# Kernel tuning notes

Hardware: AMD Instinct MI355X
Metric: run time of the kernel (lower is better)

## Reference

```python
import jax, jax.numpy as jnp
import numpy as np

B, K, IN_DIM, H, D = 8, 4096, 512, 8, 64  # batch, tokens, in_dim, heads, per-head dim


def setup_inputs() -> dict:
    key = jax.random.key(0)
    ks = jax.random.split(key, 8)
    s = 0.02
    return {
        "x": jax.random.normal(ks[0], (B, K, IN_DIM), jnp.float32),
        "y": jax.random.normal(ks[1], (B, K, IN_DIM), jnp.float32),
        "Wq": jax.random.normal(ks[2], (IN_DIM, H * D), jnp.float32) * s,
        "bq": jnp.zeros((H * D,), jnp.float32),
        "Wk": jax.random.normal(ks[3], (IN_DIM, H * D), jnp.float32) * s,
        "bk": jnp.zeros((H * D,), jnp.float32),
        "Wv": jax.random.normal(ks[4], (IN_DIM, H * D), jnp.float32) * s,
        "bv": jnp.zeros((H * D,), jnp.float32),
        "Wp": jax.random.normal(ks[5], (IN_DIM, D), jnp.float32) * s,
        "gamma": jax.random.uniform(ks[6], (H, 1, 1, 1), jnp.float32) + 0.001,
    }


def _heads(t):
    # (B, K, H*D) -> (H, B, K, D); matches split_cat(t, D, dim=2, cat dim=0) head-major layout
    b, k, _ = t.shape
    return t.reshape(b, k, H, D).transpose(2, 0, 1, 3)


def reference(x, y, Wq, bq, Wk, bk, Wv, bv, Wp, gamma):
    q = _heads(x @ Wq + bq)   # (H,B,K,D)
    kk = _heads(x @ Wk + bk)  # (H,B,K,D)
    v = _heads(y @ Wv + bv)   # (H,B,K,D)
    # energy = q^T k contracted over tokens -> (H,B,D,D)
    energy = jnp.einsum('hbkd,hbke->hbde', q, kk)
    attn = jax.nn.softmax(energy, axis=-1)
    # out = v @ attn^T : out[k,q] = sum_e v[k,e] * attn[q,e]
    out = jnp.einsum('hbke,hbqe->hbkq', v, attn)  # (H,B,K,D)
    yp = y @ Wp  # projection(y): (B,K,D)
    out = (gamma * out + yp[None]) / (1.0 + gamma)
    return out.transpose(1, 0, 2, 3)  # (B,H,K,D)
```

## Files before the change

kernel.cpp:

```cpp
#include <hip/hip_runtime.h>

#define B_ 8
#define K_ 4096
#define IN_ 512
#define H_ 8
#define D_ 64
#define HD_ 512

typedef short bf16x8 __attribute__((ext_vector_type(8)));
typedef float f32x4 __attribute__((ext_vector_type(4)));
typedef unsigned short u16;
typedef unsigned short us8v __attribute__((ext_vector_type(8)));
typedef unsigned short us4v __attribute__((ext_vector_type(4)));

__device__ inline u16 f2bf_rn(float f) {
  unsigned u = __float_as_uint(f);
  u += 0x7fffu + ((u >> 16) & 1u);
  return (u16)(u >> 16);
}
__device__ inline float bf2f(u16 h) {
  return __uint_as_float(((unsigned)h) << 16);
}

__device__ inline void gl_lds16(const u16* g, u16* l) {
  __builtin_amdgcn_global_load_lds(
      (const __attribute__((address_space(1))) unsigned int*)g,
      (__attribute__((address_space(3))) unsigned int*)l, 16, 0, 0);
}


__global__ __launch_bounds__(256) void k_cvt_x(const float* __restrict__ x,
                                               u16* __restrict__ xt_hi,
                                               u16* __restrict__ xt_lo,
                                               float* __restrict__ svec) {
  const int kt = blockIdx.x, ct = blockIdx.y, b = blockIdx.z;
  __shared__ float Xs[64][65];
  const int tid = threadIdx.x;
  const float* src = x + ((size_t)b * K_ + kt * 64) * IN_ + ct * 64;
#pragma unroll
  for (int r = 0; r < 4; ++r) {
    int idx = tid + 256 * r;
    int k = idx >> 4, c4 = (idx & 15) * 4;
    f32x4 v = *(const f32x4*)(src + (size_t)k * IN_ + c4);
    Xs[k][c4 + 0] = v[0];
    Xs[k][c4 + 1] = v[1];
    Xs[k][c4 + 2] = v[2];
    Xs[k][c4 + 3] = v[3];
  }
  __syncthreads();
  if (tid < 64) {
    float s = 0.f;
#pragma unroll
    for (int k = 0; k < 64; ++k) s += Xs[k][tid];
    atomicAdd(&svec[b * IN_ + ct * 64 + tid], s);
  }
#pragma unroll
  for (int r = 0; r < 2; ++r) {
    int idx = tid + 256 * r;
    int c = idx >> 3, ck = (idx & 7) * 8;
    us8v hv, lv;
#pragma unroll
    for (int j = 0; j < 8; ++j) {
      float f = Xs[ck + j][c];
      u16 h = f2bf_rn(f);
      float lo = f - bf2f(h);
      hv[j] = h;
      lv[j] = f2bf_rn(lo);
    }
    size_t off = ((size_t)(b * IN_ + ct * 64 + c)) * K_ + kt * 64 + ck;
    *(us8v*)(xt_hi + off) = hv;
    *(us8v*)(xt_lo + off) = lv;
  }
}

__global__ __launch_bounds__(256) void k_cvt_y(const float* __restrict__ y,
                                               u16* __restrict__ yb) {
  size_t i = ((size_t)blockIdx.x * 256 + threadIdx.x) * 8;
  f32x4 v0 = *(const f32x4*)(y + i);
  f32x4 v1 = *(const f32x4*)(y + i + 4);
  us8v o;
  o[0] = f2bf_rn(v0[0]); o[1] = f2bf_rn(v0[1]);
  o[2] = f2bf_rn(v0[2]); o[3] = f2bf_rn(v0[3]);
  o[4] = f2bf_rn(v1[0]); o[5] = f2bf_rn(v1[1]);
  o[6] = f2bf_rn(v1[2]); o[7] = f2bf_rn(v1[3]);
  *(us8v*)(yb + i) = o;
}

__global__ __launch_bounds__(256) void k_cvt_w(
    const float* __restrict__ Wq, const float* __restrict__ Wk,
    u16* __restrict__ Wqt_hi, u16* __restrict__ Wqt_lo,
    u16* __restrict__ Wkt_hi, u16* __restrict__ Wkt_lo) {
  const int ti = blockIdx.x, tj = blockIdx.y;
  const float* src = blockIdx.z ? Wk : Wq;
  u16* dhi = blockIdx.z ? Wkt_hi : Wqt_hi;
  u16* dlo = blockIdx.z ? Wkt_lo : Wqt_lo;
  __shared__ float T[64][65];
  const int tid = threadIdx.x;
#pragma unroll
  for (int r = 0; r < 4; ++r) {
    int idx = tid + 256 * r;
    int rr = idx >> 4, c4 = (idx & 15) * 4;
    f32x4 v = *(const f32x4*)(src + (size_t)(tj * 64 + rr) * 512 + ti * 64 + c4);
    T[rr][c4 + 0] = v[0]; T[rr][c4 + 1] = v[1];
    T[rr][c4 + 2] = v[2]; T[rr][c4 + 3] = v[3];
  }
  __syncthreads();
#pragma unroll
  for (int r = 0; r < 2; ++r) {
    int idx = tid + 256 * r;
    int d = idx >> 3, ck = (idx & 7) * 8;
    us8v hv, lv;
#pragma unroll
    for (int j = 0; j < 8; ++j) {
      float f = T[ck + j][d];
      u16 h = f2bf_rn(f);
      hv[j] = h;
      lv[j] = f2bf_rn(f - bf2f(h));
    }
    size_t off = (size_t)(ti * 64 + d) * 512 + tj * 64 + ck;
    *(us8v*)(dhi + off) = hv;
    *(us8v*)(dlo + off) = lv;
  }
}

#define GP 72

__global__ __launch_bounds__(256, 2) void k_gram_mfma(
    const u16* __restrict__ xt_hi, const u16* __restrict__ xt_lo,
    float* __restrict__ G) {
  const int fid = blockIdx.x;
  const int kc = fid & 7;
  const int slot = fid >> 3;
  const int b = slot / 10;
  int pp = slot - b * 10, ti = 0;
  while (pp >= 4 - ti) { pp -= 4 - ti; ++ti; }
  const int tj = ti + pp;
  const bool diag = (ti == tj);
  __shared__ u16 P[2][4 * 128 * 32];
  const int tid = threadIdx.x;
  const int wave = tid >> 6, lane = tid & 63;
  const int wm = wave & 1, wn = wave >> 1;
  const int m16 = lane & 15, quad = lane >> 4;
  const size_t base_i = ((size_t)(b * IN_ + ti * 128)) * K_;
  const size_t base_j = ((size_t)(b * IN_ + tj * 128)) * K_;
  const int sr = lane >> 2, sslot = lane & 3;
  const int boff_h = diag ? 0 : 2 * 4096;
  const int boff_l = diag ? 4096 : 3 * 4096;

  f32x4 zf = {0.f, 0.f, 0.f, 0.f};
  f32x4 acc[4][4];
#pragma unroll
  for (int mt = 0; mt < 4; ++mt)
#pragma unroll
    for (int nt = 0; nt < 4; ++nt) acc[mt][nt] = zf;
  const int kbeg = kc * 512;

  auto STAGE = [&](int t, int buf) {
    const int k0 = kbeg + t * 32;
    u16* Pb = &P[buf][0];
#pragma unroll
    for (int g = 0; g < 2; ++g) {
      int rbase = wave * 32 + g * 16;
      int r = rbase + sr;
      size_t go = (size_t)r * K_ + k0 + ((sslot ^ ((sr >> 1) & 3)) << 3);
      int lo = rbase * 32;
      gl_lds16(xt_hi + base_i + go, Pb + 0 * 4096 + lo);
      gl_lds16(xt_lo + base_i + go, Pb + 1 * 4096 + lo);
      if (!diag) {
        gl_lds16(xt_hi + base_j + go, Pb + 2 * 4096 + lo);
        gl_lds16(xt_lo + base_j + go, Pb + 3 * 4096 + lo);
      }
    }
  };

  STAGE(0, 0);
  int cur = 0;
  const int ac = ((quad ^ ((m16 >> 1) & 3)) << 3);
  for (int t = 0; t < 16; ++t) {
    if (t < 15) {
      STAGE(t + 1, cur ^ 1);
      if (diag) asm volatile("s_waitcnt vmcnt(4)" ::: "memory");
      else      asm volatile("s_waitcnt vmcnt(8)" ::: "memory");
    } else {
      asm volatile("s_waitcnt vmcnt(0)" ::: "memory");
    }
    __builtin_amdgcn_s_barrier();
    __builtin_amdgcn_sched_barrier(0);
    const u16* Pb = &P[cur][0];
    bf16x8 ah[4], al[4], bh[4], bl[4];
#pragma unroll
    for (int tt = 0; tt < 4; ++tt) {
      int ar = (wm * 64 + tt * 16 + m16) * 32 + ac;
      ah[tt] = *(const bf16x8*)(Pb + ar);
      al[tt] = *(const bf16x8*)(Pb + 4096 + ar);
      int br = (wn * 64 + tt * 16 + m16) * 32 + ac;
      bh[tt] = *(const bf16x8*)(Pb + boff_h + br);
      bl[tt] = *(const bf16x8*)(Pb + boff_l + br);
    }
#pragma unroll
    for (int mt = 0; mt < 4; ++mt)
#pragma unroll
      for (int nt = 0; nt < 4; ++nt) {
        acc[mt][nt] = __builtin_amdgcn_mfma_f32_16x16x32_bf16(
            ah[mt], bh[nt], acc[mt][nt], 0, 0, 0);
        acc[mt][nt] = __builtin_amdgcn_mfma_f32_16x16x32_bf16(
            ah[mt], bl[nt], acc[mt][nt], 0, 0, 0);
        acc[mt][nt] = __builtin_amdgcn_mfma_f32_16x16x32_bf16(
            al[mt], bh[nt], acc[mt][nt], 0, 0, 0);
      }
    __builtin_amdgcn_s_barrier();
    cur ^= 1;
  }
  float* Gb = G + (size_t)b * IN_ * IN_;
#pragma unroll
  for (int mt = 0; mt < 4; ++mt)
#pragma unroll
    for (int nt = 0; nt < 4; ++nt)
#pragma unroll
      for (int r = 0; r < 4; ++r) {
        int gi = ti * 128 + wm * 64 + mt * 16 + quad * 4 + r;
        int gj = tj * 128 + wn * 64 + nt * 16 + m16;
        atomicAdd(&Gb[(size_t)gi * IN_ + gj], acc[mt][nt][r]);
      }
}

__global__ __launch_bounds__(256) void k_cvt_g(const float* __restrict__ G,
                                               u16* __restrict__ Ghi,
                                               u16* __restrict__ Glo) {
  const int ti = blockIdx.x, tj = blockIdx.y, b = blockIdx.z;
  if (tj < ti) return;
  const float* Gb = G + (size_t)b * IN_ * IN_;
  u16* ghb = Ghi + (size_t)b * IN_ * IN_;
  u16* glb = Glo + (size_t)b * IN_ * IN_;
  __shared__ float T[64][65];
  const int tid = threadIdx.x;
#pragma unroll
  for (int r = 0; r < 4; ++r) {
    int idx = tid + 256 * r;
    int rr = idx >> 4, c4 = (idx & 15) * 4;
    f32x4 v = *(const f32x4*)(Gb + (size_t)(ti * 64 + rr) * IN_ + tj * 64 + c4);
    T[rr][c4 + 0] = v[0]; T[rr][c4 + 1] = v[1];
    T[rr][c4 + 2] = v[2]; T[rr][c4 + 3] = v[3];
  }
  __syncthreads();
#pragma unroll
  for (int r = 0; r < 2; ++r) {
    int idx = tid + 256 * r;
    int rr = idx >> 3, ck = (idx & 7) * 8;
    us8v hv, lv;
#pragma unroll
    for (int j = 0; j < 8; ++j) {
      float f = T[rr][ck + j];
      u16 h = f2bf_rn(f);
      hv[j] = h;
      lv[j] = f2bf_rn(f - bf2f(h));
    }
    size_t off = (size_t)(ti * 64 + rr) * IN_ + tj * 64 + ck;
    *(us8v*)(ghb + off) = hv;
    *(us8v*)(glb + off) = lv;
  }
  if (ti != tj) {
#pragma unroll
    for (int r = 0; r < 2; ++r) {
      int idx = tid + 256 * r;
      int rr = idx >> 3, ck = (idx & 7) * 8;
      us8v hv, lv;
#pragma unroll
      for (int j = 0; j < 8; ++j) {
        float f = T[ck + j][rr];
        u16 h = f2bf_rn(f);
        hv[j] = h;
        lv[j] = f2bf_rn(f - bf2f(h));
      }
      size_t off = (size_t)(tj * 64 + rr) * IN_ + ti * 64 + ck;
      *(us8v*)(ghb + off) = hv;
      *(us8v*)(glb + off) = lv;
    }
  }
}

__global__ __launch_bounds__(256) void k_aall_mfma(
    const u16* __restrict__ Wqt_hi, const u16* __restrict__ Wqt_lo,
    const u16* __restrict__ Ghi, const u16* __restrict__ Glo,
    u16* __restrict__ Ahi, u16* __restrict__ Alo) {
  const int ct = blockIdx.x;
  const int hb = blockIdx.y;
  const int h = hb >> 3, b = hb & 7;
  __shared__ u16 S[4 * 64 * 64];
  u16* Ah = S;
  u16* Al = S + 64 * 64;
  u16* Bh = S + 2 * 64 * 64;
  u16* Bl = S + 3 * 64 * 64;
  const int tid = threadIdx.x;
  const int wave = tid >> 6, lane = tid & 63;
  const int m16 = lane & 15, quad = lane >> 4;
  const u16* Abase_h = Wqt_hi + (size_t)(h * 64) * IN_;
  const u16* Abase_l = Wqt_lo + (size_t)(h * 64) * IN_;
  const u16* Bbase_h = Ghi + (size_t)b * IN_ * IN_ + (size_t)(ct * 64) * IN_;
  const u16* Bbase_l = Glo + (size_t)b * IN_ * IN_ + (size_t)(ct * 64) * IN_;
  const int lrow = lane >> 3;
  const int lcol = ((lane & 7) * 8) ^ (lrow << 3);
  const size_t loff = (size_t)lrow * IN_ + lcol;
  f32x4 zf = {0.f, 0.f, 0.f, 0.f};
  f32x4 acc[4] = {zf, zf, zf, zf};
  for (int k0 = 0; k0 < IN_; k0 += 64) {
    __syncthreads();
#pragma unroll
    for (int r = 0; r < 2; ++r) {
      int rg = wave * 2 + r;
      size_t go = (size_t)(rg * 8) * IN_ + k0 + loff;
      int lo = rg * 8 * 64;
      gl_lds16(Abase_h + go, &Ah[lo]);
      gl_lds16(Abase_l + go, &Al[lo]);
      gl_lds16(Bbase_h + go, &Bh[lo]);
      gl_lds16(Bbase_l + go, &Bl[lo]);
    }
    __syncthreads();
#pragma unroll
    for (int kk = 0; kk < 64; kk += 32) {
      const int ac = (kk + quad * 8) ^ ((m16 & 7) << 3);
      int arow = (wave * 16 + m16) * 64 + ac;
      bf16x8 ah = *(const bf16x8*)&Ah[arow];
      bf16x8 al = *(const bf16x8*)&Al[arow];
#pragma unroll
      for (int n = 0; n < 4; ++n) {
        int brow = (n * 16 + m16) * 64 + ac;
        bf16x8 bh = *(const bf16x8*)&Bh[brow];
        bf16x8 bl = *(const bf16x8*)&Bl[brow];
        acc[n] = __builtin_amdgcn_mfma_f32_16x16x32_bf16(ah, bh, acc[n], 0, 0, 0);
        acc[n] = __builtin_amdgcn_mfma_f32_16x16x32_bf16(ah, bl, acc[n], 0, 0, 0);
        acc[n] = __builtin_amdgcn_mfma_f32_16x16x32_bf16(al, bh, acc[n], 0, 0, 0);
      }
    }
  }
  __syncthreads();
  float* Sf = (float*)S;
#pragma unroll
  for (int n = 0; n < 4; ++n)
#pragma unroll
    for (int r = 0; r < 4; ++r) {
      int d = wave * 16 + quad * 4 + r;
      int cc = n * 16 + m16;
      Sf[d * 68 + cc] = acc[n][r];
    }
  __syncthreads();
#pragma unroll
  for (int r = 0; r < 2; ++r) {
    int idx = tid + 256 * r;
    int d = idx >> 3, ck = (idx & 7) * 8;
    us8v hv, lv;
#pragma unroll
    for (int j = 0; j < 8; ++j) {
      float f = Sf[d * 68 + ck + j];
      u16 h2 = f2bf_rn(f);
      hv[j] = h2;
      lv[j] = f2bf_rn(f - bf2f(h2));
    }
    size_t off = ((size_t)hb * 64 + d) * IN_ + ct * 64 + ck;
    *(us8v*)(Ahi + off) = hv;
    *(us8v*)(Alo + off) = lv;
  }
}

__global__ __launch_bounds__(256) void k_attn3(
    const u16* __restrict__ Ahi, const u16* __restrict__ Alo,
    const u16* __restrict__ Wqt_hi, const u16* __restrict__ Wqt_lo,
    const u16* __restrict__ Wkt_hi, const u16* __restrict__ Wkt_lo,
    const float* __restrict__ Wv, const float* __restrict__ Wp,
    const float* __restrict__ bq, const float* __restrict__ bk,
    const float* __restrict__ bv, const float* __restrict__ gamma,
    const float* __restrict__ svec, u16* __restrict__ Wft,
    float* __restrict__ bfin) {
  const int h = blockIdx.x, b = blockIdx.y;
  const int hb = h * B_ + b;
  const int tid = threadIdx.x;
  const int wave = tid >> 6, lane = tid & 63;
  const int m16 = lane & 15, quad = lane >> 4;
  __shared__ u16 S[4 * 64 * GP];
  __shared__ float Esh[64][65];
  __shared__ float t1[64], t2[64];
  u16* Ah = S;
  u16* Al = S + 64 * GP;
  u16* Bh = S + 2 * 64 * GP;
  u16* Bl = S + 3 * 64 * GP;

  if (tid < 64) {
    float s = 0.f;
    const u16* wh = Wkt_hi + (size_t)(h * 64 + tid) * IN_;
    const u16* wl = Wkt_lo + (size_t)(h * 64 + tid) * IN_;
    const float* sv = svec + b * IN_;
    for (int c = 0; c < IN_; c += 8) {
      us8v hv = *(const us8v*)(wh + c);
      us8v lv = *(const us8v*)(wl + c);
#pragma unroll
      for (int j = 0; j < 8; ++j)
        s += sv[c + j] * (bf2f(hv[j]) + bf2f(lv[j]));
    }
    t1[tid] = s;
  } else if (tid < 128) {
    int d = tid - 64;
    float s = 0.f;
    const u16* wh = Wqt_hi + (size_t)(h * 64 + d) * IN_;
    const u16* wl = Wqt_lo + (size_t)(h * 64 + d) * IN_;
    const float* sv = svec + b * IN_;
    for (int c = 0; c < IN_; c += 8) {
      us8v hv = *(const us8v*)(wh + c);
      us8v lv = *(const us8v*)(wl + c);
#pragma unroll
      for (int j = 0; j < 8; ++j)
        s += sv[c + j] * (bf2f(hv[j]) + bf2f(lv[j]));
    }
    t2[d] = s;
  }

  const u16* Abase_h = Ahi + (size_t)hb * 64 * IN_;
  const u16* Abase_l = Alo + (size_t)hb * 64 * IN_;
  const u16* Bbase_h = Wkt_hi + (size_t)(h * 64) * IN_;
  const u16* Bbase_l = Wkt_lo + (size_t)(h * 64) * IN_;
  f32x4 zf = {0.f, 0.f, 0.f, 0.f};
  f32x4 acc[4] = {zf, zf, zf, zf};
  for (int k0 = 0; k0 < IN_; k0 += 64) {
    __syncthreads();
#pragma unroll
    for (int r = 0; r < 2; ++r) {
      int idx = tid + 256 * r;
      int row = idx >> 3, ck = (idx & 7) * 8;
      int lo = row * GP + ck;
      *(us8v*)&Ah[lo] = *(const us8v*)(Abase_h + (size_t)row * IN_ + k0 + ck);
      *(us8v*)&Al[lo] = *(const us8v*)(Abase_l + (size_t)row * IN_ + k0 + ck);
      *(us8v*)&Bh[lo] = *(const us8v*)(Bbase_h + (size_t)row * IN_ + k0 + ck);
      *(us8v*)&Bl[lo] = *(const us8v*)(Bbase_l + (size_t)row * IN_ + k0 + ck);
    }
    __syncthreads();
#pragma unroll
    for (int kk = 0; kk < 64; kk += 32) {
      int arow = (wave * 16 + m16) * GP + kk + quad * 8;
      bf16x8 ah = *(const bf16x8*)&Ah[arow];
      bf16x8 al = *(const bf16x8*)&Al[arow];
#pragma unroll
      for (int n = 0; n < 4; ++n) {
        int brow = (n * 16 + m16) * GP + kk + quad * 8;
        bf16x8 bh = *(const bf16x8*)&Bh[brow];
        bf16x8 bl = *(const bf16x8*)&Bl[brow];
        acc[n] = __builtin_amdgcn_mfma_f32_16x16x32_bf16(ah, bh, acc[n], 0, 0, 0);
        acc[n] = __builtin_amdgcn_mfma_f32_16x16x32_bf16(ah, bl, acc[n], 0, 0, 0);
        acc[n] = __builtin_amdgcn_mfma_f32_16x16x32_bf16(al, bh, acc[n], 0, 0, 0);
      }
    }
  }
  __syncthreads();
#pragma unroll
  for (int n = 0; n < 4; ++n)
#pragma unroll
    for (int r = 0; r < 4; ++r) {
      int d = wave * 16 + quad * 4 + r;
      int e = n * 16 + m16;
      float bqd = bq[h * D_ + d], bke = bk[h * D_ + e];
      Esh[d][e] = acc[n][r] + bqd * t1[e] + t2[d] * bke + (float)K_ * bqd * bke;
    }
  __syncthreads();
  const float g = gamma[h];
  const float inv1g = 1.f / (1.f + g);
  if (tid < 64) {
    float m = -1e30f;
    for (int e = 0; e < 64; ++e) m = fmaxf(m, Esh[tid][e]);
    float ssum = 0.f;
    for (int e = 0; e < 64; ++e) {
      float p = __expf(Esh[tid][e] - m);
      Esh[tid][e] = p;
      ssum += p;
    }
    float inv = 1.f / ssum;
    float bsum = 0.f;
    for (int e = 0; e < 64; ++e) {
      Esh[tid][e] *= inv;
      bsum += bv[h * D_ + e] * Esh[tid][e];
    }
    bfin[hb * D_ + tid] = g * bsum * inv1g;
  }
  __syncthreads();

  bf16x8 bfr[4][2];
#pragma unroll
  for (int n = 0; n < 4; ++n)
#pragma unroll
    for (int kk = 0; kk < 2; ++kk)
#pragma unroll
      for (int j = 0; j < 8; ++j)
        bfr[n][kk][j] = f2bf_rn(Esh[n * 16 + m16][kk * 32 + quad * 8 + j]);

  u16* Wf = Wft + (size_t)hb * D_ * IN_;
#pragma unroll
  for (int mt = 0; mt < 8; ++mt) {
    f32x4 a4[4] = {zf, zf, zf, zf};
#pragma unroll
    for (int kk = 0; kk < 2; ++kk) {
      int c = wave * 128 + mt * 16 + m16;
      const float* wv = Wv + (size_t)c * HD_ + h * D_ + kk * 32 + quad * 8;
      f32x4 v0 = *(const f32x4*)wv;
      f32x4 v1 = *(const f32x4*)(wv + 4);
      bf16x8 af;
      af[0] = f2bf_rn(v0[0]); af[1] = f2bf_rn(v0[1]);
      af[2] = f2bf_rn(v0[2]); af[3] = f2bf_rn(v0[3]);
      af[4] = f2bf_rn(v1[0]); af[5] = f2bf_rn(v1[1]);
      af[6] = f2bf_rn(v1[2]); af[7] = f2bf_rn(v1[3]);
#pragma unroll
      for (int n = 0; n < 4; ++n)
        a4[n] = __builtin_amdgcn_mfma_f32_16x16x32_bf16(af, bfr[n][kk], a4[n], 0, 0, 0);
    }
    int cb = wave * 128 + mt * 16 + quad * 4;
#pragma unroll
    for (int n = 0; n < 4; ++n) {
      int q = n * 16 + m16;
      us4v st;
#pragma unroll
      for (int r = 0; r < 4; ++r) {
        float val = (g * a4[n][r] + Wp[(size_t)(cb + r) * D_ + q]) * inv1g;
        st[r] = f2bf_rn(val);
      }
      *(us4v*)(Wf + (size_t)q * IN_ + cb) = st;
    }
  }
}

__global__ __launch_bounds__(256, 2) void k_out_mfma(
    const u16* __restrict__ yb, const u16* __restrict__ Wft,
    const float* __restrict__ bfin, float* __restrict__ out) {
  const int kt = blockIdx.x;
  const int b = blockIdx.y & 7, hq = blockIdx.y >> 3;
  const int h0 = hq * 2;
  __shared__ u16 Wsh[2][2 * 64 * 64];
  const int tid = threadIdx.x, wave = tid >> 6, lane = tid & 63;
  const int m16 = lane & 15, quad = lane >> 4;
  const int swz = (m16 & 7) << 3;

  us8v stg[4];
  auto LOAD = [&](int c0) {
#pragma unroll
    for (int r = 0; r < 4; ++r) {
      int idx = tid + 256 * r;
      int row = idx >> 3, ck = (idx & 7) * 8;
      int i = row >> 6, q = row & 63;
      const u16* src =
          Wft + ((size_t)((h0 + i) * 8 + b) * 64 + q) * IN_ + c0 + ck;
      stg[r] = *(const us8v*)src;
    }
  };
  auto WRITE = [&](int buf) {
#pragma unroll
    for (int r = 0; r < 4; ++r) {
      int idx = tid + 256 * r;
      int row = idx >> 3, ck = (idx & 7) * 8;
      *(us8v*)&Wsh[buf][row * 64 + (ck ^ ((row & 7) << 3))] = stg[r];
    }
  };
  bf16x8 yf[2][4];
  auto LOADY = [&](bf16x8 (*yd)[4], int c0) {
#pragma unroll
    for (int kk = 0; kk < 2; ++kk)
#pragma unroll
      for (int ms = 0; ms < 4; ++ms) {
        int row = kt * 256 + wave * 64 + ms * 16 + m16;
        yd[kk][ms] = *(const bf16x8*)(yb + ((size_t)b * K_ + row) * IN_ + c0 +
                                      kk * 32 + quad * 8);
      }
  };

  f32x4 zf = {0.f, 0.f, 0.f, 0.f};
  f32x4 acc[4][2][4];
#pragma unroll
  for (int ms = 0; ms < 4; ++ms)
#pragma unroll
    for (int i = 0; i < 2; ++i)
#pragma unroll
      for (int nt = 0; nt < 4; ++nt) acc[ms][i][nt] = zf;

  LOAD(0);
  LOADY(yf, 0);
  WRITE(0);
  __syncthreads();
  int cur = 0;
  for (int c0 = 0; c0 < IN_; c0 += 64) {
    const bool more = (c0 + 64 < IN_);
    bf16x8 yn[2][4];
    if (more) {
      LOAD(c0 + 64);
      LOADY(yn, c0 + 64);
    }
#pragma unroll
    for (int kk = 0; kk < 2; ++kk)
#pragma unroll
      for (int i = 0; i < 2; ++i)
#pragma unroll
        for (int nt = 0; nt < 4; ++nt) {
          int brow = i * 64 + nt * 16 + m16;
          bf16x8 bb = *(const bf16x8*)&Wsh[cur][brow * 64 +
                                               ((kk * 32 + quad * 8) ^ swz)];
#pragma unroll
          for (int ms = 0; ms < 4; ++ms)
            acc[ms][i][nt] = __builtin_amdgcn_mfma_f32_16x16x32_bf16(
                yf[kk][ms], bb, acc[ms][i][nt], 0, 0, 0);
        }
    if (more) {
      WRITE(cur ^ 1);
      __syncthreads();
      cur ^= 1;
#pragma unroll
      for (int kk = 0; kk < 2; ++kk)
#pragma unroll
        for (int ms = 0; ms < 4; ++ms) yf[kk][ms] = yn[kk][ms];
    }
  }

#pragma unroll
  for (int i = 0; i < 2; ++i) {
    float* ob = out + (((size_t)b * H_ + h0 + i) * K_) * D_;
    const int hb = (h0 + i) * 8 + b;
#pragma unroll
    for (int ms = 0; ms < 4; ++ms)
#pragma unroll
      for (int nt = 0; nt < 4; ++nt) {
        int col = nt * 16 + m16;
        float bf = bfin[hb * D_ + col];
#pragma unroll
        for (int r = 0; r < 4; ++r) {
          int row = kt * 256 + wave * 64 + ms * 16 + quad * 4 + r;
          ob[(size_t)row * D_ + col] = acc[ms][i][nt][r] + bf;
        }
      }
  }
}

__global__ __launch_bounds__(256) void k_gram(const float* __restrict__ x,
                                              float* __restrict__ G,
                                              float* __restrict__ svec) {
  const int it = blockIdx.x, jt = blockIdx.y, b = blockIdx.z;
  if (jt < it) return;
  __shared__ float Xi[16][64];
  __shared__ float Xj[16][64];
  const float* Xb = x + (size_t)b * K_ * IN_;
  const int tx = threadIdx.x, ty = threadIdx.y;
  const int tid = ty * 16 + tx;
  const int i0 = it * 64, j0 = jt * 64;
  const bool diag = (it == jt);
  float acc[4][4] = {};
  float ssum = 0.f;
  for (int k0 = 0; k0 < K_; k0 += 16) {
#pragma unroll
    for (int r = 0; r < 4; ++r) {
      int idx = tid + 256 * r;
      int kk = idx >> 6, cc = idx & 63;
      const float* row = Xb + (size_t)(k0 + kk) * IN_;
      Xi[kk][cc] = row[i0 + cc];
      Xj[kk][cc] = row[j0 + cc];
    }
    __syncthreads();
#pragma unroll
    for (int kk = 0; kk < 16; ++kk) {
      float a[4], bb[4];
#pragma unroll
      for (int u = 0; u < 4; ++u) a[u] = Xi[kk][ty * 4 + u];
#pragma unroll
      for (int u = 0; u < 4; ++u) bb[u] = Xj[kk][tx * 4 + u];
#pragma unroll
      for (int u = 0; u < 4; ++u)
#pragma unroll
        for (int w = 0; w < 4; ++w) acc[u][w] += a[u] * bb[w];
    }
    if (diag && tid < 64) {
#pragma unroll
      for (int kk = 0; kk < 16; ++kk) ssum += Xi[kk][tid];
    }
    __syncthreads();
  }
  float* Gb = G + (size_t)b * IN_ * IN_;
#pragma unroll
  for (int u = 0; u < 4; ++u)
#pragma unroll
    for (int w = 0; w < 4; ++w) {
      int gi = i0 + ty * 4 + u, gj = j0 + tx * 4 + w;
      Gb[(size_t)gi * IN_ + gj] = acc[u][w];
      if (!diag) Gb[(size_t)gj * IN_ + gi] = acc[u][w];
    }
  if (diag && tid < 64) svec[b * IN_ + i0 + tid] = ssum;
}

__global__ __launch_bounds__(256) void k_aall(const float* __restrict__ Wq,
                                              const float* __restrict__ G,
                                              float* __restrict__ Aall) {
  const int jt = blockIdx.x;
  const int h = blockIdx.y, b = blockIdx.z;
  __shared__ float Ws[16][64];
  __shared__ float Gs[16][64];
  const float* Gb = G + (size_t)b * IN_ * IN_;
  const int tx = threadIdx.x, ty = threadIdx.y;
  const int tid = ty * 16 + tx;
  float acc[4][4] = {};
  for (int c0 = 0; c0 < IN_; c0 += 16) {
#pragma unroll
    for (int r = 0; r < 4; ++r) {
      int idx = tid + 256 * r;
      int kk = idx >> 6, cc = idx & 63;
      Ws[kk][cc] = Wq[(size_t)(c0 + kk) * HD_ + h * D_ + cc];
      Gs[kk][cc] = Gb[(size_t)(c0 + kk) * IN_ + jt * 64 + cc];
    }
    __syncthreads();
#pragma unroll
    for (int kk = 0; kk < 16; ++kk) {
      float a[4], bb[4];
#pragma unroll
      for (int u = 0; u < 4; ++u) a[u] = Ws[kk][ty * 4 + u];
#pragma unroll
      for (int u = 0; u < 4; ++u) bb[u] = Gs[kk][tx * 4 + u];
#pragma unroll
      for (int u = 0; u < 4; ++u)
#pragma unroll
        for (int w = 0; w < 4; ++w) acc[u][w] += a[u] * bb[w];
    }
    __syncthreads();
  }
  const int hb = h * B_ + b;
  float* Ahb = Aall + (size_t)hb * D_ * IN_;
#pragma unroll
  for (int u = 0; u < 4; ++u)
#pragma unroll
    for (int w = 0; w < 4; ++w)
      Ahb[(size_t)(ty * 4 + u) * IN_ + jt * 64 + tx * 4 + w] = acc[u][w];
}

__global__ __launch_bounds__(256) void k_attn_f32(
    const float* __restrict__ Wq, const float* __restrict__ Wk,
    const float* __restrict__ Wv, const float* __restrict__ Wp,
    const float* __restrict__ bq, const float* __restrict__ bk,
    const float* __restrict__ bv, const float* __restrict__ gamma,
    const float* __restrict__ Aall, const float* __restrict__ svec,
    float* __restrict__ Wfin, float* __restrict__ bfin) {
  const int h = blockIdx.x, b = blockIdx.y;
  const int hb = h * B_ + b;
  const int tx = threadIdx.x, ty = threadIdx.y;
  const int tid = ty * 16 + tx;
  __shared__ float Ast[64][17];
  __shared__ float Ws[16][64];
  __shared__ float Esh[64][65];
  __shared__ float t1[64], t2[64];
  const float* Ahb = Aall + (size_t)hb * D_ * IN_;
  if (tid < 64) {
    float a2 = 0.f;
    for (int c = 0; c < IN_; ++c)
      a2 += svec[b * IN_ + c] * Wk[(size_t)c * HD_ + h * D_ + tid];
    t1[tid] = a2;
  } else if (tid < 128) {
    int d = tid - 64;
    float a2 = 0.f;
    for (int c = 0; c < IN_; ++c)
      a2 += svec[b * IN_ + c] * Wq[(size_t)c * HD_ + h * D_ + d];
    t2[d] = a2;
  }
  float acc[4][4] = {};
  for (int c0 = 0; c0 < IN_; c0 += 16) {
#pragma unroll
    for (int r = 0; r < 4; ++r) {
      int idx = tid + 256 * r;
      int dd = idx >> 4, kk = idx & 15;
      Ast[dd][kk] = Ahb[(size_t)dd * IN_ + c0 + kk];
      int kk2 = idx >> 6, ee = idx & 63;
      Ws[kk2][ee] = Wk[(size_t)(c0 + kk2) * HD_ + h * D_ + ee];
    }
    __syncthreads();
#pragma unroll
    for (int kk = 0; kk < 16; ++kk) {
      float a[4], bb[4];
#pragma unroll
      for (int u = 0; u < 4; ++u) a[u] = Ast[ty * 4 + u][kk];
#pragma unroll
      for (int u = 0; u < 4; ++u) bb[u] = Ws[kk][tx * 4 + u];
#pragma unroll
      for (int u = 0; u < 4; ++u)
#pragma unroll
        for (int w = 0; w < 4; ++w) acc[u][w] += a[u] * bb[w];
    }
    __syncthreads();
  }
#pragma unroll
  for (int u = 0; u < 4; ++u) {
    int d = ty * 4 + u;
    float bqd = bq[h * D_ + d];
    float t2d = t2[d];
#pragma unroll
    for (int w = 0; w < 4; ++w) {
      int e = tx * 4 + w;
      float bke = bk[h * D_ + e];
      Esh[d][e] = acc[u][w] + bqd * t1[e] + t2d * bke + (float)K_ * bqd * bke;
    }
  }
  __syncthreads();
  if (tid < 64) {
    float m = -1e30f;
    for (int e = 0; e < 64; ++e) m = fmaxf(m, Esh[tid][e]);
    float ssum = 0.f;
    for (int e = 0; e < 64; ++e) {
      float p = __expf(Esh[tid][e] - m);
      Esh[tid][e] = p;
      ssum += p;
    }
    float inv = 1.f / ssum;
    for (int e = 0; e < 64; ++e) Esh[tid][e] *= inv;
  }
  __syncthreads();
  const float g = gamma[h];
  const float inv1g = 1.f / (1.f + g);
  if (tid < 64) {
    float a2 = 0.f;
    for (int e = 0; e < 64; ++e) a2 += bv[h * D_ + e] * Esh[tid][e];
    bfin[hb * D_ + tid] = g * a2 * inv1g;
  }
  float* Wf = Wfin + (size_t)hb * IN_ * D_;
  for (int it2 = 0; it2 < 128; ++it2) {
    int idx = tid + 256 * it2;
    int c = idx >> 6, q = idx & 63;
    const float* Wvr = Wv + (size_t)c * HD_ + h * D_;
    float a2 = 0.f;
#pragma unroll
    for (int e = 0; e < 64; ++e) a2 += Wvr[e] * Esh[q][e];
    Wf[idx] = (g * a2 + Wp[(size_t)c * D_ + q]) * inv1g;
  }
}

__global__ __launch_bounds__(256) void k_out_f32(const float* __restrict__ y,
                                                 const float* __restrict__ Wfin,
                                                 const float* __restrict__ bfin,
                                                 float* __restrict__ out) {
  const int kt = blockIdx.x;
  const int hb = blockIdx.y;
  const int h = hb >> 3, b = hb & 7;
  __shared__ float Ys[64][17];
  __shared__ float Ws[16][64];
  const int tx = threadIdx.x, ty = threadIdx.y;
  const int tid = ty * 16 + tx;
  const float* Yb = y + (size_t)b * K_ * IN_;
  const float* Wf = Wfin + (size_t)hb * IN_ * D_;
  const int k0 = kt * 64;
  float acc[4][4] = {};
  for (int c0 = 0; c0 < IN_; c0 += 16) {
#pragma unroll
    for (int r = 0; r < 4; ++r) {
      int idx = tid + 256 * r;
      int rr = idx >> 4, kk = idx & 15;
      Ys[rr][kk] = Yb[(size_t)(k0 + rr) * IN_ + c0 + kk];
      int kk2 = idx >> 6, qq = idx & 63;
      Ws[kk2][qq] = Wf[(size_t)(c0 + kk2) * D_ + qq];
    }
    __syncthreads();
#pragma unroll
    for (int kk = 0; kk < 16; ++kk) {
      float a[4], bb[4];
#pragma unroll
      for (int u = 0; u < 4; ++u) a[u] = Ys[ty * 4 + u][kk];
#pragma unroll
      for (int u = 0; u < 4; ++u) bb[u] = Ws[kk][tx * 4 + u];
#pragma unroll
      for (int u = 0; u < 4; ++u)
#pragma unroll
        for (int w = 0; w < 4; ++w) acc[u][w] += a[u] * bb[w];
    }
    __syncthreads();
  }
  float* ob = out + (((size_t)b * H_ + h) * K_ + k0) * D_;
#pragma unroll
  for (int u = 0; u < 4; ++u) {
    int k = ty * 4 + u;
#pragma unroll
    for (int w = 0; w < 4; ++w) {
      int q = tx * 4 + w;
      ob[(size_t)k * D_ + q] = acc[u][w] + bfin[hb * D_ + q];
    }
  }
}

extern "C" void kernel_launch(void* const* d_in, const int* in_sizes, int n_in,
                              void* d_out, int out_size, void* d_ws,
                              size_t ws_size, hipStream_t stream) {
  const float* x = (const float*)d_in[0];
  const float* y = (const float*)d_in[1];
  const float* Wq = (const float*)d_in[2];
  const float* bq = (const float*)d_in[3];
  const float* Wk = (const float*)d_in[4];
  const float* bk = (const float*)d_in[5];
  const float* Wv = (const float*)d_in[6];
  const float* bv = (const float*)d_in[7];
  const float* Wp = (const float*)d_in[8];
  const float* gm = (const float*)d_in[9];
  float* out = (float*)d_out;

  const size_t NEED = 86016000;
  if (ws_size >= NEED) {
    char* w = (char*)d_ws;
    u16* xt_hi = (u16*)(w);
    u16* Ahi = (u16*)(w);
    u16* Alo = (u16*)(w + 4194304);
    u16* Wft = (u16*)(w + 8388608);
    u16* xt_lo = (u16*)(w + 33554432);
    u16* yb = (u16*)(w + 33554432);
    float* G = (float*)(w + 67108864);
    u16* Ghi = (u16*)(w + 75497472);
    u16* Glo = (u16*)(w + 79691776);
    u16* Wqt_hi = (u16*)(w + 83886080);
    u16* Wqt_lo = (u16*)(w + 84410368);
    u16* Wkt_hi = (u16*)(w + 84934656);
    u16* Wkt_lo = (u16*)(w + 85458944);
    float* bfin = (float*)(w + 85983232);
    float* svec = (float*)(w + 85999616);

    hipMemsetAsync(G, 0, 8388608, stream);
    hipMemsetAsync(svec, 0, 16384, stream);
    k_cvt_w<<<dim3(8, 8, 2), 256, 0, stream>>>(Wq, Wk, Wqt_hi, Wqt_lo, Wkt_hi,
                                               Wkt_lo);
    k_cvt_x<<<dim3(64, 8, 8), 256, 0, stream>>>(x, xt_hi, xt_lo, svec);
    k_gram_mfma<<<dim3(640), 256, 0, stream>>>(xt_hi, xt_lo, G);
    k_cvt_y<<<dim3(8192), 256, 0, stream>>>(y, yb);
    k_cvt_g<<<dim3(8, 8, 8), 256, 0, stream>>>(G, Ghi, Glo);
    k_aall_mfma<<<dim3(8, 64), 256, 0, stream>>>(Wqt_hi, Wqt_lo, Ghi, Glo, Ahi,
                                                 Alo);
    k_attn3<<<dim3(8, 8), 256, 0, stream>>>(Ahi, Alo, Wqt_hi, Wqt_lo, Wkt_hi,
                                            Wkt_lo, Wv, Wp, bq, bk, bv, gm,
                                            svec, Wft, bfin);
    k_out_mfma<<<dim3(16, 32), 256, 0, stream>>>(yb, Wft, bfin, out);
  } else {
    float* ws = (float*)d_ws;
    float* G = ws;
    float* Aall = ws + 2097152;
    float* Wfin = ws + 4194304;
    float* bfin = ws + 6291456;
    float* svec = ws + 6295552;
    dim3 blk(16, 16);
    k_gram<<<dim3(8, 8, 8), blk, 0, stream>>>(x, G, svec);
    k_aall<<<dim3(8, 8, 8), blk, 0, stream>>>(Wq, G, Aall);
    k_attn_f32<<<dim3(8, 8), blk, 0, stream>>>(Wq, Wk, Wv, Wp, bq, bk, bv, gm,
                                               Aall, svec, Wfin, bfin);
    k_out_f32<<<dim3(64, 64), blk, 0, stream>>>(y, Wfin, bfin, out);
  }
}
```

Measured before the change: 328.4 us.

## Enlarge gram MFMA tiles to 256x256 with 512-thread blocks

The Gram-matrix kernel now computes 256x256 output tiles per block with 8 waves instead of 128x128 with 4 waves, cutting the grid from 640 to 192 blocks. Each wave holds 8x4 accumulator tiles and loads A fragments per row-tile inside the loop, improving operand reuse and lowering redundant global loads per output. The cost is higher register pressure, doubled LDS usage, and fewer blocks to fill the CUs, which may hurt occupancy and load balance.

```diff
diff --git a/kernel.cpp b/kernel.cpp
--- a/kernel.cpp
+++ b/kernel.cpp
@@ -125,32 +125,32 @@
 
 #define GP 72
 
-__global__ __launch_bounds__(256, 2) void k_gram_mfma(
+__global__ __launch_bounds__(512, 2) void k_gram_mfma(
     const u16* __restrict__ xt_hi, const u16* __restrict__ xt_lo,
     float* __restrict__ G) {
   const int fid = blockIdx.x;
   const int kc = fid & 7;
-  const int slot = fid >> 3;
-  const int b = slot / 10;
-  int pp = slot - b * 10, ti = 0;
-  while (pp >= 4 - ti) { pp -= 4 - ti; ++ti; }
-  const int tj = ti + pp;
+  const int sl = fid >> 3;
+  const int b = sl & 7;
+  const int pp = sl >> 3;
+  const int ti = pp >> 1, tj = (pp + 1) >> 1;
   const bool diag = (ti == tj);
-  __shared__ u16 P[2][4 * 128 * 32];
+  __shared__ u16 P[2][4 * 256 * 32];
+  const int AOFF = 256 * 32;
   const int tid = threadIdx.x;
   const int wave = tid >> 6, lane = tid & 63;
   const int wm = wave & 1, wn = wave >> 1;
   const int m16 = lane & 15, quad = lane >> 4;
-  const size_t base_i = ((size_t)(b * IN_ + ti * 128)) * K_;
-  const size_t base_j = ((size_t)(b * IN_ + tj * 128)) * K_;
+  const size_t base_i = ((size_t)(b * IN_ + ti * 256)) * K_;
+  const size_t base_j = ((size_t)(b * IN_ + tj * 256)) * K_;
   const int sr = lane >> 2, sslot = lane & 3;
-  const int boff_h = diag ? 0 : 2 * 4096;
-  const int boff_l = diag ? 4096 : 3 * 4096;
+  const int boff_h = diag ? 0 : 2 * AOFF;
+  const int boff_l = diag ? AOFF : 3 * AOFF;
 
   f32x4 zf = {0.f, 0.f, 0.f, 0.f};
-  f32x4 acc[4][4];
-#pragma unroll
-  for (int mt = 0; mt < 4; ++mt)
+  f32x4 acc[8][4];
+#pragma unroll
+  for (int mt = 0; mt < 8; ++mt)
 #pragma unroll
     for (int nt = 0; nt < 4; ++nt) acc[mt][nt] = zf;
   const int kbeg = kc * 512;
@@ -164,11 +164,11 @@
       int r = rbase + sr;
       size_t go = (size_t)r * K_ + k0 + ((sslot ^ ((sr >> 1) & 3)) << 3);
       int lo = rbase * 32;
-      gl_lds16(xt_hi + base_i + go, Pb + 0 * 4096 + lo);
-      gl_lds16(xt_lo + base_i + go, Pb + 1 * 4096 + lo);
+      gl_lds16(xt_hi + base_i + go, Pb + lo);
+      gl_lds16(xt_lo + base_i + go, Pb + AOFF + lo);
       if (!diag) {
-        gl_lds16(xt_hi + base_j + go, Pb + 2 * 4096 + lo);
-        gl_lds16(xt_lo + base_j + go, Pb + 3 * 4096 + lo);
+        gl_lds16(xt_hi + base_j + go, Pb + 2 * AOFF + lo);
+        gl_lds16(xt_lo + base_j + go, Pb + 3 * AOFF + lo);
       }
     }
   };
@@ -187,39 +187,40 @@
     __builtin_amdgcn_s_barrier();
     __builtin_amdgcn_sched_barrier(0);
     const u16* Pb = &P[cur][0];
-    bf16x8 ah[4], al[4], bh[4], bl[4];
-#pragma unroll
-    for (int tt = 0; tt < 4; ++tt) {
-      int ar = (wm * 64 + tt * 16 + m16) * 32 + ac;
-      ah[tt] = *(const bf16x8*)(Pb + ar);
-      al[tt] = *(const bf16x8*)(Pb + 4096 + ar);
-      int br = (wn * 64 + tt * 16 + m16) * 32 + ac;
-      bh[tt] = *(const bf16x8*)(Pb + boff_h + br);
-      bl[tt] = *(const bf16x8*)(Pb + boff_l + br);
-    }
-#pragma unroll
-    for (int mt = 0; mt < 4; ++mt)
+    bf16x8 bh[4], bl[4];
+#pragma unroll
+    for (int nt = 0; nt < 4; ++nt) {
+      int br = (wn * 64 + nt * 16 + m16) * 32 + ac;
+      bh[nt] = *(const bf16x8*)(Pb + boff_h + br);
+      bl[nt] = *(const bf16x8*)(Pb + boff_l + br);
+    }
+#pragma unroll
+    for (int mt = 0; mt < 8; ++mt) {
+      int ar = (wm * 128 + mt * 16 + m16) * 32 + ac;
+      bf16x8 ah = *(const bf16x8*)(Pb + ar);
+      bf16x8 al = *(const bf16x8*)(Pb + AOFF + ar);
 #pragma unroll
       for (int nt = 0; nt < 4; ++nt) {
         acc[mt][nt] = __builtin_amdgcn_mfma_f32_16x16x32_bf16(
-            ah[mt], bh[nt], acc[mt][nt], 0, 0, 0);
+            ah, bh[nt], acc[mt][nt], 0, 0, 0);
         acc[mt][nt] = __builtin_amdgcn_mfma_f32_16x16x32_bf16(
-            ah[mt], bl[nt], acc[mt][nt], 0, 0, 0);
+            ah, bl[nt], acc[mt][nt], 0, 0, 0);
         acc[mt][nt] = __builtin_amdgcn_mfma_f32_16x16x32_bf16(
-            al[mt], bh[nt], acc[mt][nt], 0, 0, 0);
+            al, bh[nt], acc[mt][nt], 0, 0, 0);
       }
+    }
     __builtin_amdgcn_s_barrier();
     cur ^= 1;
   }
   float* Gb = G + (size_t)b * IN_ * IN_;
 #pragma unroll
-  for (int mt = 0; mt < 4; ++mt)
+  for (int mt = 0; mt < 8; ++mt)
 #pragma unroll
     for (int nt = 0; nt < 4; ++nt)
 #pragma unroll
       for (int r = 0; r < 4; ++r) {
-        int gi = ti * 128 + wm * 64 + mt * 16 + quad * 4 + r;
-        int gj = tj * 128 + wn * 64 + nt * 16 + m16;
+        int gi = ti * 256 + wm * 128 + mt * 16 + quad * 4 + r;
+        int gj = tj * 256 + wn * 64 + nt * 16 + m16;
         atomicAdd(&Gb[(size_t)gi * IN_ + gj], acc[mt][nt][r]);
       }
 }
@@ -916,7 +917,7 @@
     k_cvt_w<<<dim3(8, 8, 2), 256, 0, stream>>>(Wq, Wk, Wqt_hi, Wqt_lo, Wkt_hi,
                                                Wkt_lo);
     k_cvt_x<<<dim3(64, 8, 8), 256, 0, stream>>>(x, xt_hi, xt_lo, svec);
-    k_gram_mfma<<<dim3(640), 256, 0, stream>>>(xt_hi, xt_lo, G);
+    k_gram_mfma<<<dim3(192), 512, 0, stream>>>(xt_hi, xt_lo, G);
     k_cvt_y<<<dim3(8192), 256, 0, stream>>>(y, yb);
     k_cvt_g<<<dim3(8, 8, 8), 256, 0, stream>>>(G, Ghi, Glo);
     k_aall_mfma<<<dim3(8, 64), 256, 0, stream>>>(Wqt_hi, Wqt_lo, Ghi, Glo, Ahi,
```

Measured after the change: 348.9 us. 1.06x slower.

## Split final weight fusion out of attention kernel into wider-grid k_wft

Applied to the files above, without the earlier changes.

The attention kernel now stops after the softmax and writes the bf16 attention matrix to workspace, reusing the Gram buffer region. A new kernel k_wft with a 4x64 grid computes the fused Wv·attn plus Wp weight matrix, splitting the 512 output columns across four blocks per head-batch pair. The aim is to spread the serial MFMA tail, which previously ran on only 64 blocks, across more CUs. The cost is an extra launch plus a small global round trip for the attention matrix.

```diff
diff --git a/kernel.cpp b/kernel.cpp
--- a/kernel.cpp
+++ b/kernel.cpp
@@ -366,10 +366,9 @@
     const u16* __restrict__ Ahi, const u16* __restrict__ Alo,
     const u16* __restrict__ Wqt_hi, const u16* __restrict__ Wqt_lo,
     const u16* __restrict__ Wkt_hi, const u16* __restrict__ Wkt_lo,
-    const float* __restrict__ Wv, const float* __restrict__ Wp,
     const float* __restrict__ bq, const float* __restrict__ bk,
     const float* __restrict__ bv, const float* __restrict__ gamma,
-    const float* __restrict__ svec, u16* __restrict__ Wft,
+    const float* __restrict__ svec, u16* __restrict__ Pbf,
     float* __restrict__ bfin) {
   const int h = blockIdx.x, b = blockIdx.y;
   const int hb = h * B_ + b;
@@ -480,22 +479,49 @@
   }
   __syncthreads();
 
+  {
+    int q = tid >> 2, c0 = (tid & 3) * 16;
+    us8v o1, o2;
+#pragma unroll
+    for (int j = 0; j < 8; ++j) {
+      o1[j] = f2bf_rn(Esh[q][c0 + j]);
+      o2[j] = f2bf_rn(Esh[q][c0 + 8 + j]);
+    }
+    u16* Pq = Pbf + (size_t)hb * 4096 + q * 64 + c0;
+    *(us8v*)Pq = o1;
+    *(us8v*)(Pq + 8) = o2;
+  }
+}
+
+__global__ __launch_bounds__(256) void k_wft(
+    const u16* __restrict__ Pbf, const float* __restrict__ Wv,
+    const float* __restrict__ Wp, const float* __restrict__ gamma,
+    u16* __restrict__ Wft) {
+  const int ct = blockIdx.x;
+  const int hb = blockIdx.y;
+  const int h = hb >> 3;
+  const int tid = threadIdx.x, wave = tid >> 6, lane = tid & 63;
+  const int m16 = lane & 15, quad = lane >> 4;
+  const float g = gamma[h];
+  const float inv1g = 1.f / (1.f + g);
+  f32x4 zf = {0.f, 0.f, 0.f, 0.f};
+
   bf16x8 bfr[4][2];
+  const u16* Pb = Pbf + (size_t)hb * 4096;
 #pragma unroll
   for (int n = 0; n < 4; ++n)
 #pragma unroll
     for (int kk = 0; kk < 2; ++kk)
-#pragma unroll
-      for (int j = 0; j < 8; ++j)
-        bfr[n][kk][j] = f2bf_rn(Esh[n * 16 + m16][kk * 32 + quad * 8 + j]);
+      bfr[n][kk] =
+          *(const bf16x8*)(Pb + (n * 16 + m16) * 64 + kk * 32 + quad * 8);
 
   u16* Wf = Wft + (size_t)hb * D_ * IN_;
 #pragma unroll
-  for (int mt = 0; mt < 8; ++mt) {
+  for (int mt = 0; mt < 2; ++mt) {
     f32x4 a4[4] = {zf, zf, zf, zf};
 #pragma unroll
     for (int kk = 0; kk < 2; ++kk) {
-      int c = wave * 128 + mt * 16 + m16;
+      int c = ct * 128 + wave * 32 + mt * 16 + m16;
       const float* wv = Wv + (size_t)c * HD_ + h * D_ + kk * 32 + quad * 8;
       f32x4 v0 = *(const f32x4*)wv;
       f32x4 v1 = *(const f32x4*)(wv + 4);
@@ -508,7 +534,7 @@
       for (int n = 0; n < 4; ++n)
         a4[n] = __builtin_amdgcn_mfma_f32_16x16x32_bf16(af, bfr[n][kk], a4[n], 0, 0, 0);
     }
-    int cb = wave * 128 + mt * 16 + quad * 4;
+    int cb = ct * 128 + wave * 32 + mt * 16 + quad * 4;
 #pragma unroll
     for (int n = 0; n < 4; ++n) {
       int q = n * 16 + m16;
@@ -902,6 +928,7 @@
     u16* xt_lo = (u16*)(w + 33554432);
     u16* yb = (u16*)(w + 33554432);
     float* G = (float*)(w + 67108864);
+    u16* Pbf = (u16*)(w + 67108864);
     u16* Ghi = (u16*)(w + 75497472);
     u16* Glo = (u16*)(w + 79691776);
     u16* Wqt_hi = (u16*)(w + 83886080);
@@ -922,8 +949,9 @@
     k_aall_mfma<<<dim3(8, 64), 256, 0, stream>>>(Wqt_hi, Wqt_lo, Ghi, Glo, Ahi,
                                                  Alo);
     k_attn3<<<dim3(8, 8), 256, 0, stream>>>(Ahi, Alo, Wqt_hi, Wqt_lo, Wkt_hi,
-                                            Wkt_lo, Wv, Wp, bq, bk, bv, gm,
-                                            svec, Wft, bfin);
+                                            Wkt_lo, bq, bk, bv, gm, svec, Pbf,
+                                            bfin);
+    k_wft<<<dim3(4, 64), 256, 0, stream>>>(Pbf, Wv, Wp, gm, Wft);
     k_out_mfma<<<dim3(16, 32), 256, 0, stream>>>(yb, Wft, bfin, out);
   } else {
     float* ws = (float*)d_ws;
```

Measured after the change: 325.8 us (median of 2 runs). About the same (-0.8%).
